# Kernel optimization log

Hardware: AMD Instinct MI355X
Metric: run time of the kernel (lower is better)

Reference implementation:

```python
import jax, jax.numpy as jnp
import numpy as np

VX, VY = 0.2, 0.2
X_OFF = VX / 2 + 0.0          # vx/2 + pc_range[0]
Y_OFF = VY / 2 + (-40.0)      # vy/2 + pc_range[1]
K = 8                          # hardcoded in GCNLayer
BN_EPS = 1e-3
LRELU_SLOPE = 0.2
V, T, C_IN, C_OUT = 4096, 100, 4, 64


def _gcn_layer(x, conv_w, bn_gamma, bn_beta, bn_mean, bn_var):
    """DGCNN EdgeConv layer. x: [N, T, C]. Returns [N, T, O]."""
    N, Tn, C = x.shape
    # KNN on negative squared distance (self included in topk, as in torch code)
    xx = jnp.sum(x * x, axis=-1)                       # [N, T]
    inner = jnp.einsum('ntc,nsc->nts', x, x)           # [N, T, T]
    neg_dist = 2.0 * inner - xx[:, :, None] - xx[:, None, :]
    _, idx = jax.lax.top_k(neg_dist, K)                # [N, T, K]
    # gather neighbor features: nbr[n,t,k,c] = x[n, idx[n,t,k], c]
    nbr = x[jnp.arange(N)[:, None, None], idx]         # [N, T, K, C]
    xc = x[:, :, None, :]                              # [N, T, 1, C]
    edge = jnp.concatenate(
        [nbr - xc, jnp.broadcast_to(xc, (N, Tn, K, C))], axis=-1)  # [N,T,K,2C]
    # 1x1 conv (no bias) + eval-mode BatchNorm + LeakyReLU(0.2)
    h = jnp.einsum('ntkc,oc->ntko', edge, conv_w)      # [N, T, K, O]
    scale = bn_gamma / jnp.sqrt(bn_var + BN_EPS)
    h = (h - bn_mean) * scale + bn_beta
    h = jax.nn.leaky_relu(h, LRELU_SLOPE)
    return jnp.max(h, axis=2)                          # max over k -> [N, T, O]


def setup_inputs() -> dict:
    key = jax.random.key(0)
    k1, k2, k3, k4, k5, k6 = jax.random.split(key, 6)
    features = jax.random.normal(k1, (V, T, C_IN), dtype=jnp.float32)
    num_voxels = jnp.maximum(
        jax.random.randint(k2, (V,), 0, T), 1).astype(jnp.int32)
    coors = jax.random.randint(k3, (V, 4), 0, 352).astype(jnp.int32)
    # GCNLayer params: Conv2d(18, 64, 1, bias=False) + BatchNorm2d(64)
    conv_w = jax.random.normal(k4, (C_OUT, 18), dtype=jnp.float32) * 0.1
    bn_gamma = jnp.ones((C_OUT,), jnp.float32)
    bn_beta = jnp.zeros((C_OUT,), jnp.float32)
    bn_mean = jax.random.normal(k5, (C_OUT,), jnp.float32) * 0.1
    bn_var = 1.0 + 0.1 * jax.random.uniform(k6, (C_OUT,), jnp.float32)
    return {"features": features, "conv_w": conv_w, "bn_gamma": bn_gamma,
            "bn_beta": bn_beta, "bn_mean": bn_mean, "bn_var": bn_var,
            "num_voxels": num_voxels, "coors": coors}


def reference(features, conv_w, bn_gamma, bn_beta, bn_mean, bn_var,
              num_voxels, coors):
    nv = num_voxels.astype(features.dtype)
    # decorate: cluster offsets (xyz - mean) and pillar-center offsets (xy)
    points_mean = jnp.sum(features[:, :, :3], axis=1, keepdims=True) / nv[:, None, None]
    f_cluster = features[:, :, :3] - points_mean                      # [V,T,3]
    fx = features[:, :, 0] - (coors[:, 3].astype(features.dtype)[:, None] * VX + X_OFF)
    fy = features[:, :, 1] - (coors[:, 2].astype(features.dtype)[:, None] * VY + Y_OFF)
    f_center = jnp.stack([fx, fy], axis=-1)                           # [V,T,2]
    feat = jnp.concatenate([features, f_cluster, f_center], axis=-1)  # [V,T,9]
    # padding mask: point t valid iff t < num_voxels[v]
    mask = (jnp.arange(T)[None, :] < num_voxels[:, None]).astype(features.dtype)
    feat = feat * mask[:, :, None]
    # single GCN (last) layer; batch_process chunking is a no-op mathematically
    out = _gcn_layer(feat, conv_w, bn_gamma, bn_beta, bn_mean, bn_var)  # [V,T,64]
    out = out * mask[:, :, None]            # (+ zeros prev_features_out)
    out = jnp.max(out, axis=1)              # max over points -> [V, 64]
    return out
```

## Files before the change

### kernel.cpp

```cpp
#include <hip/hip_runtime.h>

#define TPTS 100
#define CO   64
#define KK   8
#define NW   8

__device__ __forceinline__ unsigned umin_(unsigned a, unsigned b) { return a < b ? a : b; }
__device__ __forceinline__ unsigned umax_(unsigned a, unsigned b) { return a > b ? a : b; }
__device__ __forceinline__ _Float16 hmax_(_Float16 a, _Float16 b) { return a > b ? a : b; }

__device__ __forceinline__ unsigned med3u(unsigned a, unsigned b, unsigned c) {
    unsigned d;
    asm("v_med3_u32 %0, %1, %2, %3" : "=v"(d) : "v"(a), "v"(b), "v"(c));
    return d;
}

__device__ __forceinline__ unsigned dist_key(const float4 qt, const float4 qs, unsigned s) {
    float dx = qt.x - qs.x, dy = qt.y - qs.y;
    float dz = qt.z - qs.z, dw = qt.w - qs.w;
    float e = __fmaf_rn(dx, dx, __fmaf_rn(dy, dy, __fmaf_rn(dz, dz, dw * dw)));
    return (__float_as_uint(e) & 0xFFFFFF80u) | s;
}

__device__ __forceinline__ void ins8(unsigned val[KK], unsigned key) {
    #pragma unroll
    for (int k = KK - 1; k >= 1; --k)
        val[k] = med3u(val[k - 1], val[k], key);
    val[0] = umin_(val[0], key);
}

__global__ __launch_bounds__(512) void dgcnn_kernel(
    const float* __restrict__ features,
    const float* __restrict__ conv_w,
    const float* __restrict__ bn_gamma,
    const float* __restrict__ bn_beta,
    const float* __restrict__ bn_mean,
    const float* __restrict__ bn_var,
    const int*  __restrict__ num_voxels,
    const int*  __restrict__ coors,
    float* __restrict__ out)
{
    __shared__ float    s_feat[TPTS][12];
    __shared__ float    s_xx[TPTS];
    __shared__ unsigned s_idxp[TPTS][2];
    __shared__ float    s_red[NW][CO];
    __shared__ float    s_mean[4];
    __shared__ union {
        float    stage[TPTS][4];
        _Float16 g16[TPTS][CO];
    } s_u;

    const float INF = __builtin_inff();
    const int v   = blockIdx.x;
    const int tid = threadIdx.x;
    const int nv  = num_voxels[v];

    float4 f = make_float4(0.f, 0.f, 0.f, 0.f);
    if (tid < TPTS) {
        f = reinterpret_cast<const float4*>(features)[v * TPTS + tid];
        *reinterpret_cast<float4*>(&s_u.stage[tid][0]) = f;
    }
    __syncthreads();

    if (tid < 96) {
        int ch = tid >> 5, j = tid & 31;
        float p = s_u.stage[j][ch] + s_u.stage[j + 32][ch] + s_u.stage[j + 64][ch];
        if (j < 4) p += s_u.stage[j + 96][ch];
        #pragma unroll
        for (int off = 16; off >= 1; off >>= 1)
            p += __shfl_xor(p, off, 32);
        if (j == 0) s_mean[ch] = p / (float)nv;
    }
    __syncthreads();

    if (tid < TPTS) {
        float mask = (tid < nv) ? 1.0f : 0.0f;
        float c3 = (float)coors[v * 4 + 3];
        float c2 = (float)coors[v * 4 + 2];
        float r0 = f.x * mask, r1 = f.y * mask, r2 = f.z * mask, r3 = f.w * mask;
        float r4 = (f.x - s_mean[0]) * mask;
        float r5 = (f.y - s_mean[1]) * mask;
        float r6 = (f.z - s_mean[2]) * mask;
        float r7 = (f.x - (c3 * 0.2f + 0.1f)) * mask;
        float r8 = (f.y - (c2 * 0.2f - 39.9f)) * mask;
        float xx = r0*r0 + r1*r1 + r2*r2 + r3*r3 + r4*r4
                 + r5*r5 + r6*r6 + r7*r7 + r8*r8;
        float4* rowv = reinterpret_cast<float4*>(&s_feat[tid][0]);
        rowv[0] = make_float4(1.7320508075688772f * r0,
                              1.7320508075688772f * r1,
                              1.4142135623730951f * r2, r3);
        rowv[1] = make_float4(r4, r5, r6, r7);
        rowv[2] = make_float4(r8, 0.f, 0.f, 0.f);
        s_xx[tid] = xx;
    }

    const int o  = tid & 63;
    const int wv = tid >> 6;
    const float sgn = (bn_gamma[o] < 0.f) ? -1.f : 1.f;
    float w1[9], w2[9];
    #pragma unroll
    for (int c = 0; c < 9; ++c) {
        const float ws = (c == 0 || c == 1) ? 0.57735026918962576f
                       : (c == 2) ? 0.70710678118654752f : 1.f;
        float a = conv_w[o * 18 + c];
        float b = conv_w[o * 18 + 9 + c];
        w1[c] = a * sgn * ws;
        w2[c] = (b - a) * sgn * ws;
    }
    __syncthreads();

    const int nd = (nv + 31) >> 5;

    {
        int r0 = nv + wv;
        if (r0 < TPTS) s_u.g16[r0][o] = (_Float16)0.f;
    }

    if (wv < nd) {
        const int trow = wv * 32 + (o & 31);
        const int bsd  = o >> 5;
        if (trow < nv) {
            const float4 qt = *reinterpret_cast<const float4*>(&s_feat[trow][0]);
            unsigned val[KK];
            #pragma unroll
            for (int k = 0; k < KK; ++k) val[k] = 0xFFFFFFFFu;
            int mcnt = TPTS - nv; if (mcnt > KK) mcnt = KK;
            int ha = (nv + mcnt + 1) >> 1; if (ha > nv) ha = nv;
            int s        = bsd ? ha : 0;
            const int se = bsd ? nv : ha;
            #pragma unroll 2
            for (; s < se; ++s) {
                const float4 qs = *reinterpret_cast<const float4*>(&s_feat[s][0]);
                ins8(val, dist_key(qt, qs, (unsigned)s));
            }
            if (bsd) {
                unsigned kmb = __float_as_uint(s_xx[trow]) & 0xFFFFFF80u;
                for (int j = 0; j < mcnt; ++j)
                    ins8(val, kmb | (unsigned)(nv + j));
            }
            unsigned other[KK];
            #pragma unroll
            for (int k = 0; k < KK; ++k) other[k] = __shfl_xor(val[k], 32);
            if (!bsd) {
                unsigned m[KK];
                #pragma unroll
                for (int k = 0; k < KK; ++k)
                    m[k] = umin_(val[k], other[KK - 1 - k]) & 127u;
                unsigned p0 = m[0] | (m[1] << 8) | (m[2] << 16) | (m[3] << 24);
                unsigned p1 = m[4] | (m[5] << 8) | (m[6] << 16) | (m[7] << 24);
                *reinterpret_cast<uint2*>(&s_idxp[trow][0]) = make_uint2(p0, p1);
            }
        }
    } else {
        const int step = NW - nd;
        for (int sR = wv - nd; sR < nv; sR += step) {
            const float4* row = reinterpret_cast<const float4*>(&s_feat[sR][0]);
            float4 a = row[0], b = row[1];
            float c8 = s_feat[sR][8];
            float g = a.x * w1[0];
            g = __fmaf_rn(a.y, w1[1], g);
            g = __fmaf_rn(a.z, w1[2], g);
            g = __fmaf_rn(a.w, w1[3], g);
            g = __fmaf_rn(b.x, w1[4], g);
            g = __fmaf_rn(b.y, w1[5], g);
            g = __fmaf_rn(b.z, w1[6], g);
            g = __fmaf_rn(b.w, w1[7], g);
            g = __fmaf_rn(c8,  w1[8], g);
            s_u.g16[sR][o] = (_Float16)g;
        }
    }
    __syncthreads();

    float acc = -INF;
    for (int tt = wv; tt < nv; tt += NW) {
        const float4* row = reinterpret_cast<const float4*>(&s_feat[tt][0]);
        float4 a = row[0], b = row[1];
        float c8 = s_feat[tt][8];
        float base = a.x * w2[0];
        base = __fmaf_rn(a.y, w2[1], base);
        base = __fmaf_rn(a.z, w2[2], base);
        base = __fmaf_rn(a.w, w2[3], base);
        base = __fmaf_rn(b.x, w2[4], base);
        base = __fmaf_rn(b.y, w2[5], base);
        base = __fmaf_rn(b.z, w2[6], base);
        base = __fmaf_rn(b.w, w2[7], base);
        base = __fmaf_rn(c8,  w2[8], base);
        uint2 pk = *reinterpret_cast<const uint2*>(&s_idxp[tt][0]);
        int i0 =  pk.x        & 255, i1 = (pk.x >>  8) & 255;
        int i2 = (pk.x >> 16) & 255, i3 = (pk.x >> 24) & 255;
        int i4 =  pk.y        & 255, i5 = (pk.y >>  8) & 255;
        int i6 = (pk.y >> 16) & 255, i7 = (pk.y >> 24) & 255;
        _Float16 g0 = s_u.g16[i0][o], g1 = s_u.g16[i1][o];
        _Float16 g2 = s_u.g16[i2][o], g3 = s_u.g16[i3][o];
        _Float16 g4 = s_u.g16[i4][o], g5 = s_u.g16[i5][o];
        _Float16 g6 = s_u.g16[i6][o], g7 = s_u.g16[i7][o];
        _Float16 gm = hmax_(hmax_(hmax_(g0, g1), hmax_(g2, g3)),
                            hmax_(hmax_(g4, g5), hmax_(g6, g7)));
        acc = fmaxf(acc, (float)gm + base);
    }
    s_red[wv][o] = acc;
    __syncthreads();

    if (tid < CO) {
        float m = s_red[0][tid];
        #pragma unroll
        for (int i = 1; i < NW; ++i) m = fmaxf(m, s_red[i][tid]);
        float scale = bn_gamma[tid] / sqrtf(bn_var[tid] + 0.001f);
        float bias  = bn_beta[tid] - bn_mean[tid] * scale;
        float h = m * fabsf(scale) + bias;
        float a = (h > 0.f) ? h : 0.2f * h;
        if (nv < TPTS) a = fmaxf(a, 0.f);
        out[v * CO + tid] = a;
    }
}

extern "C" void kernel_launch(void* const* d_in, const int* in_sizes, int n_in,
                              void* d_out, int out_size, void* d_ws, size_t ws_size,
                              hipStream_t stream) {
    const float* features = (const float*)d_in[0];
    const float* conv_w   = (const float*)d_in[1];
    const float* bn_gamma = (const float*)d_in[2];
    const float* bn_beta  = (const float*)d_in[3];
    const float* bn_mean  = (const float*)d_in[4];
    const float* bn_var   = (const float*)d_in[5];
    const int*   num_vox  = (const int*)d_in[6];
    const int*   coor     = (const int*)d_in[7];
    float* outp = (float*)d_out;
    const int V = in_sizes[6];
    dgcnn_kernel<<<V, 512, 0, stream>>>(features, conv_w, bn_gamma, bn_beta,
                                        bn_mean, bn_var, num_vox, coor, outp);
}
```

Measured before the change: 108.3 us.

## Fold derived feature channels into 4-wide weights and shrink shared memory

The derived channels (cluster offsets and pillar-center offsets) are affine in the raw 4 features. The change folds them into combined 4-element weights plus a per-voxel constant, so only a 4-float row per point is stored in shared memory. The per-point conv projections drop from 9 FMAs to 4, and LDS use falls because the 12-float rows are gone and the reduction buffer now shares the union. An extra barrier is needed before reusing the union for the reduction. Folding the weights also slightly changes float rounding.

```diff
diff --git a/kernel.cpp b/kernel.cpp
--- a/kernel.cpp
+++ b/kernel.cpp
@@ -6,7 +6,6 @@
 #define NW   8
 
 __device__ __forceinline__ unsigned umin_(unsigned a, unsigned b) { return a < b ? a : b; }
-__device__ __forceinline__ unsigned umax_(unsigned a, unsigned b) { return a > b ? a : b; }
 __device__ __forceinline__ _Float16 hmax_(_Float16 a, _Float16 b) { return a > b ? a : b; }
 
 __device__ __forceinline__ unsigned med3u(unsigned a, unsigned b, unsigned c) {
@@ -40,14 +39,14 @@
     const int*  __restrict__ coors,
     float* __restrict__ out)
 {
-    __shared__ float    s_feat[TPTS][12];
+    __shared__ float    s_q[TPTS][4];
     __shared__ float    s_xx[TPTS];
     __shared__ unsigned s_idxp[TPTS][2];
-    __shared__ float    s_red[NW][CO];
     __shared__ float    s_mean[4];
     __shared__ union {
         float    stage[TPTS][4];
         _Float16 g16[TPTS][CO];
+        float    red[NW][CO];
     } s_u;
 
     const float INF = __builtin_inff();
@@ -73,40 +72,50 @@
     }
     __syncthreads();
 
+    const float cx = (float)coors[v * 4 + 3] * 0.2f + 0.1f;
+    const float cy = (float)coors[v * 4 + 2] * 0.2f - 39.9f;
+    const float m0 = s_mean[0], m1 = s_mean[1], m2 = s_mean[2];
+
     if (tid < TPTS) {
         float mask = (tid < nv) ? 1.0f : 0.0f;
-        float c3 = (float)coors[v * 4 + 3];
-        float c2 = (float)coors[v * 4 + 2];
         float r0 = f.x * mask, r1 = f.y * mask, r2 = f.z * mask, r3 = f.w * mask;
-        float r4 = (f.x - s_mean[0]) * mask;
-        float r5 = (f.y - s_mean[1]) * mask;
-        float r6 = (f.z - s_mean[2]) * mask;
-        float r7 = (f.x - (c3 * 0.2f + 0.1f)) * mask;
-        float r8 = (f.y - (c2 * 0.2f - 39.9f)) * mask;
+        float r4 = (f.x - m0) * mask;
+        float r5 = (f.y - m1) * mask;
+        float r6 = (f.z - m2) * mask;
+        float r7 = (f.x - cx) * mask;
+        float r8 = (f.y - cy) * mask;
         float xx = r0*r0 + r1*r1 + r2*r2 + r3*r3 + r4*r4
                  + r5*r5 + r6*r6 + r7*r7 + r8*r8;
-        float4* rowv = reinterpret_cast<float4*>(&s_feat[tid][0]);
-        rowv[0] = make_float4(1.7320508075688772f * r0,
-                              1.7320508075688772f * r1,
-                              1.4142135623730951f * r2, r3);
-        rowv[1] = make_float4(r4, r5, r6, r7);
-        rowv[2] = make_float4(r8, 0.f, 0.f, 0.f);
+        *reinterpret_cast<float4*>(&s_q[tid][0]) =
+            make_float4(1.7320508075688772f * r0,
+                        1.7320508075688772f * r1,
+                        1.4142135623730951f * r2, r3);
         s_xx[tid] = xx;
     }
 
     const int o  = tid & 63;
     const int wv = tid >> 6;
     const float sgn = (bn_gamma[o] < 0.f) ? -1.f : 1.f;
-    float w1[9], w2[9];
+    float w1r[9], w2r[9];
     #pragma unroll
     for (int c = 0; c < 9; ++c) {
-        const float ws = (c == 0 || c == 1) ? 0.57735026918962576f
-                       : (c == 2) ? 0.70710678118654752f : 1.f;
         float a = conv_w[o * 18 + c];
         float b = conv_w[o * 18 + 9 + c];
-        w1[c] = a * sgn * ws;
-        w2[c] = (b - a) * sgn * ws;
-    }
+        w1r[c] = a * sgn;
+        w2r[c] = (b - a) * sgn;
+    }
+    const float i3 = 0.57735026918962576f, i2 = 0.70710678118654752f;
+    float wq1[4], wq2[4];
+    wq1[0] = (w1r[0] + w1r[4] + w1r[7]) * i3;
+    wq1[1] = (w1r[1] + w1r[5] + w1r[8]) * i3;
+    wq1[2] = (w1r[2] + w1r[6]) * i2;
+    wq1[3] = w1r[3];
+    wq2[0] = (w2r[0] + w2r[4] + w2r[7]) * i3;
+    wq2[1] = (w2r[1] + w2r[5] + w2r[8]) * i3;
+    wq2[2] = (w2r[2] + w2r[6]) * i2;
+    wq2[3] = w2r[3];
+    const float c1v = -(w1r[4]*m0 + w1r[5]*m1 + w1r[6]*m2 + w1r[7]*cx + w1r[8]*cy);
+    const float c2v = -(w2r[4]*m0 + w2r[5]*m1 + w2r[6]*m2 + w2r[7]*cx + w2r[8]*cy);
     __syncthreads();
 
     const int nd = (nv + 31) >> 5;
@@ -120,7 +129,7 @@
         const int trow = wv * 32 + (o & 31);
         const int bsd  = o >> 5;
         if (trow < nv) {
-            const float4 qt = *reinterpret_cast<const float4*>(&s_feat[trow][0]);
+            const float4 qt = *reinterpret_cast<const float4*>(&s_q[trow][0]);
             unsigned val[KK];
             #pragma unroll
             for (int k = 0; k < KK; ++k) val[k] = 0xFFFFFFFFu;
@@ -130,7 +139,7 @@
             const int se = bsd ? nv : ha;
             #pragma unroll 2
             for (; s < se; ++s) {
-                const float4 qs = *reinterpret_cast<const float4*>(&s_feat[s][0]);
+                const float4 qs = *reinterpret_cast<const float4*>(&s_q[s][0]);
                 ins8(val, dist_key(qt, qs, (unsigned)s));
             }
             if (bsd) {
@@ -154,18 +163,12 @@
     } else {
         const int step = NW - nd;
         for (int sR = wv - nd; sR < nv; sR += step) {
-            const float4* row = reinterpret_cast<const float4*>(&s_feat[sR][0]);
-            float4 a = row[0], b = row[1];
-            float c8 = s_feat[sR][8];
-            float g = a.x * w1[0];
-            g = __fmaf_rn(a.y, w1[1], g);
-            g = __fmaf_rn(a.z, w1[2], g);
-            g = __fmaf_rn(a.w, w1[3], g);
-            g = __fmaf_rn(b.x, w1[4], g);
-            g = __fmaf_rn(b.y, w1[5], g);
-            g = __fmaf_rn(b.z, w1[6], g);
-            g = __fmaf_rn(b.w, w1[7], g);
-            g = __fmaf_rn(c8,  w1[8], g);
+            const float4 q = *reinterpret_cast<const float4*>(&s_q[sR][0]);
+            float g = c1v;
+            g = __fmaf_rn(q.x, wq1[0], g);
+            g = __fmaf_rn(q.y, wq1[1], g);
+            g = __fmaf_rn(q.z, wq1[2], g);
+            g = __fmaf_rn(q.w, wq1[3], g);
             s_u.g16[sR][o] = (_Float16)g;
         }
     }
@@ -173,38 +176,33 @@
 
     float acc = -INF;
     for (int tt = wv; tt < nv; tt += NW) {
-        const float4* row = reinterpret_cast<const float4*>(&s_feat[tt][0]);
-        float4 a = row[0], b = row[1];
-        float c8 = s_feat[tt][8];
-        float base = a.x * w2[0];
-        base = __fmaf_rn(a.y, w2[1], base);
-        base = __fmaf_rn(a.z, w2[2], base);
-        base = __fmaf_rn(a.w, w2[3], base);
-        base = __fmaf_rn(b.x, w2[4], base);
-        base = __fmaf_rn(b.y, w2[5], base);
-        base = __fmaf_rn(b.z, w2[6], base);
-        base = __fmaf_rn(b.w, w2[7], base);
-        base = __fmaf_rn(c8,  w2[8], base);
+        const float4 q = *reinterpret_cast<const float4*>(&s_q[tt][0]);
+        float base = c2v;
+        base = __fmaf_rn(q.x, wq2[0], base);
+        base = __fmaf_rn(q.y, wq2[1], base);
+        base = __fmaf_rn(q.z, wq2[2], base);
+        base = __fmaf_rn(q.w, wq2[3], base);
         uint2 pk = *reinterpret_cast<const uint2*>(&s_idxp[tt][0]);
         int i0 =  pk.x        & 255, i1 = (pk.x >>  8) & 255;
-        int i2 = (pk.x >> 16) & 255, i3 = (pk.x >> 24) & 255;
+        int i2 = (pk.x >> 16) & 255, i3_ = (pk.x >> 24) & 255;
         int i4 =  pk.y        & 255, i5 = (pk.y >>  8) & 255;
         int i6 = (pk.y >> 16) & 255, i7 = (pk.y >> 24) & 255;
         _Float16 g0 = s_u.g16[i0][o], g1 = s_u.g16[i1][o];
-        _Float16 g2 = s_u.g16[i2][o], g3 = s_u.g16[i3][o];
+        _Float16 g2 = s_u.g16[i2][o], g3 = s_u.g16[i3_][o];
         _Float16 g4 = s_u.g16[i4][o], g5 = s_u.g16[i5][o];
         _Float16 g6 = s_u.g16[i6][o], g7 = s_u.g16[i7][o];
         _Float16 gm = hmax_(hmax_(hmax_(g0, g1), hmax_(g2, g3)),
                             hmax_(hmax_(g4, g5), hmax_(g6, g7)));
         acc = fmaxf(acc, (float)gm + base);
     }
-    s_red[wv][o] = acc;
+    __syncthreads();
+    s_u.red[wv][o] = acc;
     __syncthreads();
 
     if (tid < CO) {
-        float m = s_red[0][tid];
+        float m = s_u.red[0][tid];
         #pragma unroll
-        for (int i = 1; i < NW; ++i) m = fmaxf(m, s_red[i][tid]);
+        for (int i = 1; i < NW; ++i) m = fmaxf(m, s_u.red[i][tid]);
         float scale = bn_gamma[tid] / sqrtf(bn_var[tid] + 0.001f);
         float bias  = bn_beta[tid] - bn_mean[tid] * scale;
         float h = m * fabsf(scale) + bias;
```

Measured after the change: 108.0 us. Within noise of the previous version (-0.2%).
